# Kernel tuning notes

Measured on AMD Instinct MI355X. Metric: run time of the kernel, lower is better.

The kernel has to match this reference:

```python
import jax, jax.numpy as jnp
import numpy as np

B, T, C, HR = 8, 4096, 256, 4
N_LAYER, LAYER_ID = 12, 3
HID = HR * C


def _fancy_decay_first():
    # Faithful reproduction of VRWKV_SpatialMix._init_weights(init_mode='fancy')
    r01 = LAYER_ID / (N_LAYER - 1)
    h = np.arange(C, dtype=np.float32)
    decay = -5.0 + 8.0 * (h / (C - 1)) ** (0.7 + 1.3 * r01)
    zig = ((np.arange(1, C + 1) % 3) - 1).astype(np.float32) * 0.5
    first = np.float32(np.log(0.3)) + zig
    return jnp.asarray(decay, jnp.float32), jnp.asarray(first, jnp.float32)


def setup_inputs() -> dict:
    key = jax.random.key(0)
    ks = jax.random.split(key, 12)
    s = 0.02  # small weight scale keeps exp(k) well-conditioned
    decay, first = _fancy_decay_first()
    return {
        "x": jax.random.normal(ks[0], (B, T, C), jnp.float32),
        "Wk": jax.random.normal(ks[1], (C, C), jnp.float32) * s,
        "Wv": jax.random.normal(ks[2], (C, C), jnp.float32) * s,
        "Wr": jax.random.normal(ks[3], (C, C), jnp.float32) * s,
        "Wo": jax.random.normal(ks[4], (C, C), jnp.float32) * s,
        "Wk_ffn": jax.random.normal(ks[5], (C, HID), jnp.float32) * s,
        "Wv_ffn": jax.random.normal(ks[6], (HID, C), jnp.float32) * s,
        "Wr_ffn": jax.random.normal(ks[7], (C, C), jnp.float32) * s,
        "g1": 1.0 + 0.1 * jax.random.normal(ks[8], (C,), jnp.float32),
        "b1": 0.1 * jax.random.normal(ks[9], (C,), jnp.float32),
        "g2": 1.0 + 0.1 * jax.random.normal(ks[10], (C,), jnp.float32),
        "b2": 0.1 * jax.random.normal(ks[11], (C,), jnp.float32),
        "spatial_decay": decay,
        "spatial_first": first,
    }


def _ln(x, g, b):
    m = jnp.mean(x, axis=-1, keepdims=True)
    v = jnp.var(x, axis=-1, keepdims=True)
    return (x - m) * jax.lax.rsqrt(v + 1e-5) * g + b


def _wkv(w, u, k, v):
    # Numerically-stable log-space WKV recurrence (same math as wkv_cuda):
    # y_t = (sum_{i<t} e^{w*(t-1-i)+k_i} v_i + e^{u+k_t} v_t)
    #     / (sum_{i<t} e^{w*(t-1-i)+k_i}     + e^{u+k_t})
    # w,u: [C]; k,v: [B,T,C] -> y: [B,T,C]
    Bb, Tt, Cc = k.shape
    kT = jnp.swapaxes(k, 0, 1)  # [T,B,C]
    vT = jnp.swapaxes(v, 0, 1)

    def step(carry, kv):
        p, q, o = carry           # [B,C] num / den / running max exponent
        kt, vt = kv               # [B,C]
        no = jnp.maximum(o, u + kt)
        A = jnp.exp(o - no)
        E = jnp.exp(u + kt - no)
        y = (A * p + E * vt) / (A * q + E)
        no2 = jnp.maximum(w + o, kt)
        A2 = jnp.exp(w + o - no2)
        E2 = jnp.exp(kt - no2)
        return (A2 * p + E2 * vt, A2 * q + E2, no2), y

    init = (jnp.zeros((Bb, Cc), k.dtype),
            jnp.zeros((Bb, Cc), k.dtype),
            jnp.full((Bb, Cc), -1e38, k.dtype))
    _, yT = jax.lax.scan(step, init, (kT, vT))
    return jnp.swapaxes(yT, 0, 1)


def reference(x, Wk, Wv, Wr, Wo, Wk_ffn, Wv_ffn, Wr_ffn, g1, b1, g2, b2,
              spatial_decay, spatial_first):
    Tlen = x.shape[1]
    # --- SpatialMix (shift_pixel=0 -> xk=xv=xr=h, key_norm=False) ---
    h = _ln(x, g1, b1)
    k = h @ Wk
    v = h @ Wv
    sr = jax.nn.sigmoid(h @ Wr)
    y = _wkv(spatial_decay / Tlen, spatial_first / Tlen, k, v)
    x = x + (sr * y) @ Wo
    # --- ChannelMix (square-ReLU MLP, sigmoid receptance gate) ---
    h2 = _ln(x, g2, b2)
    kk = jnp.square(jax.nn.relu(h2 @ Wk_ffn))
    x = x + jax.nn.sigmoid(h2 @ Wr_ffn) * (kk @ Wv_ffn)
    return x
```

## Files before the change

kernel.cpp:

```cpp
#include <hip/hip_runtime.h>
#include <hip/hip_bf16.h>
#include <math.h>

#define TDIM 4096
#define CDIM 256
#define BDIM 8
#define NTOK (BDIM * TDIM)
#define HIDDIM 1024
#define NCHUNK 256
#define CHLEN 16

typedef float f32x4 __attribute__((ext_vector_type(4)));
typedef __bf16 bf16x8 __attribute__((ext_vector_type(8)));
typedef __bf16 bf16x4 __attribute__((ext_vector_type(4)));
typedef long long i64x2 __attribute__((ext_vector_type(2)));

#define GLDS16(gp, lp) __builtin_amdgcn_global_load_lds( \
    (const __attribute__((address_space(1))) void*)(gp), \
    (__attribute__((address_space(3))) void*)(lp), 16, 0, 0)

#define WAITCNT_VM5  0x0F75
#define WAITCNT_VM4  0x0F74
#define WAITCNT_VM0  0x0F70

__device__ __forceinline__ float sigm(float v) { return 1.0f / (1.0f + __expf(-v)); }

__device__ __forceinline__ int permk(int k) {
  return (k & ~63) + (((k >> 3) & 3) << 4) + (((k >> 5) & 1) << 3) + (k & 7);
}

__global__ __launch_bounds__(256) void pack_weights(
    const float* __restrict__ Wk, const float* __restrict__ Wv,
    const float* __restrict__ Wr, const float* __restrict__ Wo,
    const float* __restrict__ Wkf, const float* __restrict__ Wvf,
    const float* __restrict__ Wrf,
    __bf16* __restrict__ WoT, unsigned char* __restrict__ Wkvr8,
    unsigned char* __restrict__ Wkfr8, unsigned char* __restrict__ Wvf8) {
  long long j = (long long)blockIdx.x * 256 + threadIdx.x;
  if (j < 49152) {
    const long long d = j * 4;
    const int n = (int)(d >> 8), k0 = (int)(d & 255);
    const float* src = (n < 256) ? Wk : (n < 512 ? Wv : Wr);
    const int nn = n & 255;
    int w = 0;
    w = __builtin_amdgcn_cvt_pk_fp8_f32(src[k0 * 256 + nn],
                                        src[(k0 + 1) * 256 + nn], w, false);
    w = __builtin_amdgcn_cvt_pk_fp8_f32(src[(k0 + 2) * 256 + nn],
                                        src[(k0 + 3) * 256 + nn], w, true);
    *(int*)&Wkvr8[(long long)n * 256 + permk(k0)] = w;
    return;
  }
  j -= 49152;
  if (j < 65536) { int n = (int)(j >> 8), k = (int)(j & 255);
    WoT[j] = (__bf16)Wo[k * 256 + n]; return; }
  j -= 65536;
  if (j < 81920) {
    const long long d = j * 4;
    const int n = (int)(d >> 8), k0 = (int)(d & 255);
    float v0, v1, v2, v3;
    if (n < 1024) {
      v0 = Wkf[(long long)k0 * 1024 + n];       v1 = Wkf[(long long)(k0 + 1) * 1024 + n];
      v2 = Wkf[(long long)(k0 + 2) * 1024 + n]; v3 = Wkf[(long long)(k0 + 3) * 1024 + n];
    } else {
      const int m = n - 1024;
      v0 = Wrf[k0 * 256 + m];       v1 = Wrf[(k0 + 1) * 256 + m];
      v2 = Wrf[(k0 + 2) * 256 + m]; v3 = Wrf[(k0 + 3) * 256 + m];
    }
    int w = 0;
    w = __builtin_amdgcn_cvt_pk_fp8_f32(v0, v1, w, false);
    w = __builtin_amdgcn_cvt_pk_fp8_f32(v2, v3, w, true);
    *(int*)&Wkfr8[(long long)n * 256 + permk(k0)] = w;
    return;
  }
  j -= 81920;
  if (j < 65536) {
    const long long d = j * 4;
    const int n = (int)(d >> 10), k0 = (int)(d & 1023);
    int w = 0;
    w = __builtin_amdgcn_cvt_pk_fp8_f32(Wvf[(long long)k0 * 256 + n],
                                        Wvf[(long long)(k0 + 1) * 256 + n], w, false);
    w = __builtin_amdgcn_cvt_pk_fp8_f32(Wvf[(long long)(k0 + 2) * 256 + n],
                                        Wvf[(long long)(k0 + 3) * 256 + n], w, true);
    *(int*)&Wvf8[(long long)n * 1024 + permk(k0)] = w;
    return;
  }
}

__global__ __launch_bounds__(256) void ln_kernel(
    const float* __restrict__ x, const float* __restrict__ gamma,
    const float* __restrict__ beta, unsigned char* __restrict__ h8) {
  const int wave = threadIdx.x >> 6, lane = threadIdx.x & 63;
  const long long row = (long long)blockIdx.x * 4 + wave;
  const long long base = row * CDIM + lane * 4;
  const f32x4 v = *(const f32x4*)&x[base];
  float s = v[0] + v[1] + v[2] + v[3];
  float s2 = v[0]*v[0] + v[1]*v[1] + v[2]*v[2] + v[3]*v[3];
  #pragma unroll
  for (int o = 1; o < 64; o <<= 1) { s += __shfl_xor(s, o); s2 += __shfl_xor(s2, o); }
  const float mean = s * (1.0f / CDIM);
  const float var = s2 * (1.0f / CDIM) - mean * mean;
  const float rstd = rsqrtf(var + 1e-5f);
  const f32x4 g4 = *(const f32x4*)&gamma[lane * 4];
  const f32x4 b4 = *(const f32x4*)&beta[lane * 4];
  float o0 = (v[0] - mean) * rstd * g4[0] + b4[0];
  float o1 = (v[1] - mean) * rstd * g4[1] + b4[1];
  float o2 = (v[2] - mean) * rstd * g4[2] + b4[2];
  float o3 = (v[3] - mean) * rstd * g4[3] + b4[3];
  int w = 0;
  w = __builtin_amdgcn_cvt_pk_fp8_f32(o0, o1, w, false);
  w = __builtin_amdgcn_cvt_pk_fp8_f32(o2, o3, w, true);
  *(int*)&h8[row * CDIM + permk(lane * 4)] = w;
}

template <int K, int EPI>
__global__ __launch_bounds__(256, 3) void gemm9(
    const unsigned char* __restrict__ A8, const unsigned char* __restrict__ B8,
    int M, __bf16* __restrict__ outH, __bf16* __restrict__ outH2,
    unsigned char* __restrict__ outC,
    float* __restrict__ outF, const __bf16* __restrict__ srcH,
    const __bf16* __restrict__ gate) {
  constexpr int NIT = K / 64;
  __shared__ unsigned char sA[3][128 * 64];
  __shared__ unsigned char sB[3][128 * 64];
  const int tid = threadIdx.x;
  const int wave = tid >> 6, lane = tid & 63;
  const int quad = lane >> 4, mrow = lane & 15;
  const long long bm = (long long)blockIdx.x * 128;
  const long long bn = (long long)blockIdx.y * 128;
  const int wm = (wave & 1) * 64, wn = (wave >> 1) * 64;
  const int srow = lane >> 2;
  const int o16 = (lane & 3) * 16;

  auto issue = [&](int g) {
    const int buf = g % 3;
    const long long k0 = (long long)g * 64;
    const int a0 = wave * 32;
    GLDS16(A8 + (bm + a0 + srow) * (long long)K + k0 + o16, &sA[buf][a0 * 64]);
    GLDS16(A8 + (bm + a0 + 16 + srow) * (long long)K + k0 + o16, &sA[buf][(a0 + 16) * 64]);
    GLDS16(B8 + (bn + a0 + srow) * (long long)K + k0 + o16, &sB[buf][a0 * 64]);
    GLDS16(B8 + (bn + a0 + 16 + srow) * (long long)K + k0 + o16, &sB[buf][(a0 + 16) * 64]);
  };

  f32x4 acc[4][4] = {};
  issue(0);
  if (NIT > 1) issue(1);

  auto compute = [&](int g) {
    const int buf = g % 3;
    i64x2 fa[4], fb[4];
    #pragma unroll
    for (int mt = 0; mt < 4; mt++)
      fa[mt] = *(const i64x2*)&sA[buf][(wm + mt * 16 + mrow) * 64 + quad * 16];
    #pragma unroll
    for (int nt = 0; nt < 4; nt++)
      fb[nt] = *(const i64x2*)&sB[buf][(wn + nt * 16 + mrow) * 64 + quad * 16];
    #pragma unroll
    for (int c = 0; c < 2; c++)
      #pragma unroll
      for (int mt = 0; mt < 4; mt++)
        #pragma unroll
        for (int nt = 0; nt < 4; nt++)
          acc[mt][nt] = __builtin_amdgcn_mfma_f32_16x16x32_fp8_fp8(
              fb[nt][c], fa[mt][c], acc[mt][nt], 0, 0, 0);
  };

  #pragma unroll 1
  for (int g = 0; g < NIT; g++) {
    if (g == NIT - 1) {
      __builtin_amdgcn_s_waitcnt(WAITCNT_VM0);
    } else {
      __builtin_amdgcn_s_waitcnt(WAITCNT_VM4);
    }
    __builtin_amdgcn_s_barrier();
    if (g + 2 < NIT) issue(g + 2);
    compute(g);
  }

  #pragma unroll
  for (int mt = 0; mt < 4; mt++) {
    #pragma unroll
    for (int nt = 0; nt < 4; nt++) {
      const long long row = bm + wm + mt * 16 + mrow;
      const long long colb = bn + wn + nt * 16 + quad * 4;
      const f32x4 a = acc[mt][nt];
      if (EPI == 0) {
        const int plane = blockIdx.y >> 1;
        __bf16* o = outH + (long long)plane * ((long long)M * 256);
        const long long c2 = colb & 255;
        bf16x4 v;
        if (plane == 2) {
          #pragma unroll
          for (int r = 0; r < 4; r++) v[r] = (__bf16)sigm(a[r]);
        } else {
          #pragma unroll
          for (int r = 0; r < 4; r++) v[r] = (__bf16)a[r];
        }
        *(bf16x4*)&o[row * 256 + c2] = v;
      } else if (EPI == 2) {
        if (blockIdx.y < 8) {
          float t0 = a[0] > 0.0f ? a[0] : 0.0f;
          float t1 = a[1] > 0.0f ? a[1] : 0.0f;
          float t2 = a[2] > 0.0f ? a[2] : 0.0f;
          float t3 = a[3] > 0.0f ? a[3] : 0.0f;
          int w = 0;
          w = __builtin_amdgcn_cvt_pk_fp8_f32(t0 * t0, t1 * t1, w, false);
          w = __builtin_amdgcn_cvt_pk_fp8_f32(t2 * t2, t3 * t3, w, true);
          *(int*)&outC[row * 1024 + permk((int)colb)] = w;
        } else {
          bf16x4 v;
          #pragma unroll
          for (int r = 0; r < 4; r++) v[r] = (__bf16)sigm(a[r]);
          *(bf16x4*)&outH2[row * 256 + (colb - 1024)] = v;
        }
      } else {
        const long long idx = row * 256 + colb;
        const bf16x4 s4 = *(const bf16x4*)&srcH[idx];
        const bf16x4 g4 = *(const bf16x4*)&gate[idx];
        f32x4 v;
        #pragma unroll
        for (int r = 0; r < 4; r++) v[r] = (float)s4[r] + (float)g4[r] * a[r];
        *(f32x4*)&outF[idx] = v;
      }
    }
  }
}

__global__ __launch_bounds__(256, 2) void gemm7(
    const __bf16* __restrict__ A, const __bf16* __restrict__ Bt,
    const float* __restrict__ x,
    const float* __restrict__ gammaP, const float* __restrict__ betaP,
    __bf16* __restrict__ x1h, unsigned char* __restrict__ h28) {
  constexpr int K = 256;
  __shared__ __bf16 sA[3][64 * 32];
  __shared__ __bf16 sB[3][256 * 32];
  __shared__ float redS[4][64], redQ[4][64];

  const int tid = threadIdx.x;
  const int wave = tid >> 6, lane = tid & 63;
  const int quad = lane >> 4, mrow = lane & 15;
  const long long bm = (long long)blockIdx.x * 64;
  const int wn = wave * 64;
  const int lrow = lane >> 2;
  const int lk = (lane & 3) * 8;

  auto issue = [&](int g) {
    const int buf = g % 3;
    const long long k0 = (long long)g * 32;
    GLDS16(A + (bm + wave * 16 + lrow) * (long long)K + k0 + lk,
           &sA[buf][(wave * 16) * 32]);
    #pragma unroll
    for (int bc = 0; bc < 4; bc++) {
      const int r0 = wave * 64 + bc * 16;
      GLDS16(Bt + (r0 + lrow) * (long long)K + k0 + lk, &sB[buf][r0 * 32]);
    }
  };

  f32x4 acc[4][4] = {};

  auto compute = [&](int g) {
    const int buf = g % 3;
    bf16x8 fa[4], fb[4];
    #pragma unroll
    for (int mt = 0; mt < 4; mt++)
      fa[mt] = *(const bf16x8*)&sA[buf][(mt * 16 + mrow) * 32 + quad * 8];
    #pragma unroll
    for (int nt = 0; nt < 4; nt++)
      fb[nt] = *(const bf16x8*)&sB[buf][(wn + nt * 16 + mrow) * 32 + quad * 8];
    #pragma unroll
    for (int mt = 0; mt < 4; mt++)
      #pragma unroll
      for (int nt = 0; nt < 4; nt++)
        acc[mt][nt] = __builtin_amdgcn_mfma_f32_16x16x32_bf16(fb[nt], fa[mt], acc[mt][nt], 0, 0, 0);
  };

  issue(0);
  issue(1);
  #pragma unroll 1
  for (int g = 0; g < 8; g++) {
    if (g == 7) {
      __builtin_amdgcn_s_waitcnt(WAITCNT_VM0);
    } else {
      __builtin_amdgcn_s_waitcnt(WAITCNT_VM5);
    }
    __builtin_amdgcn_s_barrier();
    if (g + 2 < 8) issue(g + 2);
    compute(g);
  }

  float sum[4] = {0, 0, 0, 0}, sq[4] = {0, 0, 0, 0};
  #pragma unroll
  for (int mt = 0; mt < 4; mt++) {
    #pragma unroll
    for (int nt = 0; nt < 4; nt++) {
      const long long row = bm + mt * 16 + mrow;
      const long long colb = wn + nt * 16 + quad * 4;
      acc[mt][nt] += *(const f32x4*)&x[row * 256 + colb];
      #pragma unroll
      for (int r = 0; r < 4; r++) {
        sum[mt] += acc[mt][nt][r];
        sq[mt] += acc[mt][nt][r] * acc[mt][nt][r];
      }
    }
  }
  #pragma unroll
  for (int mt = 0; mt < 4; mt++) {
    sum[mt] += __shfl_xor(sum[mt], 16); sq[mt] += __shfl_xor(sq[mt], 16);
    sum[mt] += __shfl_xor(sum[mt], 32); sq[mt] += __shfl_xor(sq[mt], 32);
  }
  if (quad == 0) {
    #pragma unroll
    for (int mt = 0; mt < 4; mt++) {
      redS[wave][mt * 16 + mrow] = sum[mt];
      redQ[wave][mt * 16 + mrow] = sq[mt];
    }
  }
  __syncthreads();
  #pragma unroll
  for (int mt = 0; mt < 4; mt++) {
    const int rb = mt * 16 + mrow;
    const float ts = redS[0][rb] + redS[1][rb] + redS[2][rb] + redS[3][rb];
    const float tq = redQ[0][rb] + redQ[1][rb] + redQ[2][rb] + redQ[3][rb];
    const float mean = ts * (1.0f / 256.0f);
    const float rstd = rsqrtf(tq * (1.0f / 256.0f) - mean * mean + 1e-5f);
    const long long row = bm + rb;
    #pragma unroll
    for (int nt = 0; nt < 4; nt++) {
      const long long colb = wn + nt * 16 + quad * 4;
      const f32x4 g4 = *(const f32x4*)&gammaP[colb];
      const f32x4 b4 = *(const f32x4*)&betaP[colb];
      bf16x4 xo;
      const float t0 = acc[mt][nt][0], t1 = acc[mt][nt][1];
      const float t2 = acc[mt][nt][2], t3 = acc[mt][nt][3];
      xo[0] = (__bf16)t0; xo[1] = (__bf16)t1; xo[2] = (__bf16)t2; xo[3] = (__bf16)t3;
      const float h0 = (t0 - mean) * rstd * g4[0] + b4[0];
      const float h1 = (t1 - mean) * rstd * g4[1] + b4[1];
      const float h2v = (t2 - mean) * rstd * g4[2] + b4[2];
      const float h3 = (t3 - mean) * rstd * g4[3] + b4[3];
      *(bf16x4*)&x1h[row * 256 + colb] = xo;
      int w = 0;
      w = __builtin_amdgcn_cvt_pk_fp8_f32(h0, h1, w, false);
      w = __builtin_amdgcn_cvt_pk_fp8_f32(h2v, h3, w, true);
      *(int*)&h28[row * 256 + permk((int)colb)] = w;
    }
  }
}

__global__ __launch_bounds__(256) void wkv_phase1(
    const __bf16* __restrict__ ka, const __bf16* __restrict__ va,
    const float* __restrict__ decay,
    float* __restrict__ Sloc, float* __restrict__ Zloc) {
  const int wave = threadIdx.x >> 6, lane = threadIdx.x & 63;
  const int gi = blockIdx.x * 4 + wave;
  const int b = gi >> 8, chunk = gi & (NCHUNK - 1);
  const int c0 = lane * 4;
  const f32x4 w4 = *(const f32x4*)&decay[c0];
  f32x4 ew;
  #pragma unroll
  for (int r = 0; r < 4; r++) ew[r] = __expf(w4[r] * (1.0f / TDIM));
  f32x4 S = {0,0,0,0}, Z = {0,0,0,0};
  long long base = ((long long)b * TDIM + (long long)chunk * CHLEN) * 256 + c0;
  #pragma unroll 4
  for (int t = 0; t < CHLEN; t++) {
    const bf16x4 k4 = *(const bf16x4*)&ka[base + (long long)t * 256];
    const bf16x4 v4 = *(const bf16x4*)&va[base + (long long)t * 256];
    #pragma unroll
    for (int r = 0; r < 4; r++) {
      const float ek = __expf((float)k4[r]);
      S[r] = ew[r] * S[r] + ek * (float)v4[r];
      Z[r] = ew[r] * Z[r] + ek;
    }
  }
  const long long o = (long long)gi * 256 + c0;
  *(f32x4*)&Sloc[o] = S;
  *(f32x4*)&Zloc[o] = Z;
}

__global__ __launch_bounds__(256) void wkv_phase2(
    const float* __restrict__ Sloc, const float* __restrict__ Zloc,
    const float* __restrict__ decay,
    float* __restrict__ Sstart, float* __restrict__ Zstart) {
  const int idx = blockIdx.x * 256 + threadIdx.x;
  const int c = idx & 255;
  const int b = idx >> 8;
  const float w = decay[c] * (1.0f / TDIM);
  const float ewL = __expf(w * (float)CHLEN);
  float S = 0.0f, Z = 0.0f;
  for (int j = 0; j < NCHUNK; j++) {
    const long long o = ((long long)b * NCHUNK + j) * 256 + c;
    Sstart[o] = S;
    Zstart[o] = Z;
    S = ewL * S + Sloc[o];
    Z = ewL * Z + Zloc[o];
  }
}

__global__ __launch_bounds__(256) void wkv_phase3(
    const __bf16* __restrict__ ka, const __bf16* __restrict__ va,
    const __bf16* __restrict__ ra,
    const float* __restrict__ decay, const float* __restrict__ first,
    const float* __restrict__ Sstart, const float* __restrict__ Zstart,
    __bf16* __restrict__ a2) {
  const int wave = threadIdx.x >> 6, lane = threadIdx.x & 63;
  const int gi = blockIdx.x * 4 + wave;
  const int b = gi >> 8, chunk = gi & (NCHUNK - 1);
  const int c0 = lane * 4;
  const f32x4 w4 = *(const f32x4*)&decay[c0];
  const f32x4 u4 = *(const f32x4*)&first[c0];
  f32x4 ew, eu;
  #pragma unroll
  for (int r = 0; r < 4; r++) {
    ew[r] = __expf(w4[r] * (1.0f / TDIM));
    eu[r] = __expf(u4[r] * (1.0f / TDIM));
  }
  const long long so = (long long)gi * 256 + c0;
  f32x4 S = *(const f32x4*)&Sstart[so];
  f32x4 Z = *(const f32x4*)&Zstart[so];
  long long base = ((long long)b * TDIM + (long long)chunk * CHLEN) * 256 + c0;
  #pragma unroll 2
  for (int t = 0; t < CHLEN; t++) {
    const long long p = base + (long long)t * 256;
    const bf16x4 k4 = *(const bf16x4*)&ka[p];
    const bf16x4 v4 = *(const bf16x4*)&va[p];
    const bf16x4 r4 = *(const bf16x4*)&ra[p];
    bf16x4 o;
    #pragma unroll
    for (int r = 0; r < 4; r++) {
      const float ek = __expf((float)k4[r]);
      const float E = eu[r] * ek;
      const float y = (S[r] + E * (float)v4[r]) / (Z[r] + E);
      o[r] = (__bf16)((float)r4[r] * y);
      S[r] = ew[r] * S[r] + ek * (float)v4[r];
      Z[r] = ew[r] * Z[r] + ek;
    }
    *(bf16x4*)&a2[p] = o;
  }
}

extern "C" void kernel_launch(void* const* d_in, const int* in_sizes, int n_in,
                              void* d_out, int out_size, void* d_ws, size_t ws_size,
                              hipStream_t stream) {
  const float* x     = (const float*)d_in[0];
  const float* Wk    = (const float*)d_in[1];
  const float* Wv    = (const float*)d_in[2];
  const float* Wr    = (const float*)d_in[3];
  const float* Wo    = (const float*)d_in[4];
  const float* Wkf   = (const float*)d_in[5];
  const float* Wvf   = (const float*)d_in[6];
  const float* Wrf   = (const float*)d_in[7];
  const float* g1    = (const float*)d_in[8];
  const float* b1    = (const float*)d_in[9];
  const float* g2    = (const float*)d_in[10];
  const float* b2    = (const float*)d_in[11];
  const float* decay = (const float*)d_in[12];
  const float* first = (const float*)d_in[13];
  float* out = (float*)d_out;
  char* ws = (char*)d_ws;

  __bf16* ka     = (__bf16*)(ws + 0);
  __bf16* va     = (__bf16*)(ws + 16777216LL);
  __bf16* ra     = (__bf16*)(ws + 33554432LL);
  __bf16* a2     = (__bf16*)(ws + 50331648LL);
  __bf16* g2buf  = (__bf16*)(ws + 50331648LL);
  unsigned char* h8  = (unsigned char*)(ws + 67108864LL);
  unsigned char* h28 = (unsigned char*)(ws + 67108864LL);
  __bf16* x1h    = (__bf16*)(ws + 83886080LL);
  unsigned char* kk8 = (unsigned char*)(ws + 100663296LL);
  float*  Sloc   = (float*)(ws + 134217728LL);
  float*  Zloc   = (float*)(ws + 137363456LL);
  float*  Sstart = (float*)(ws + 140509184LL);
  float*  Zstart = (float*)(ws + 143654912LL);
  __bf16* WoT    = (__bf16*)(ws + 167772160LL);
  unsigned char* Wkvr8 = (unsigned char*)(ws + 167903232LL);
  unsigned char* Wkfr8 = (unsigned char*)(ws + 168099840LL);
  unsigned char* Wvf8  = (unsigned char*)(ws + 168427520LL);

  pack_weights<<<1024, 256, 0, stream>>>(Wk, Wv, Wr, Wo, Wkf, Wvf, Wrf,
                                         WoT, Wkvr8, Wkfr8, Wvf8);

  ln_kernel<<<NTOK / 4, 256, 0, stream>>>(x, g1, b1, h8);
  gemm9<256, 0><<<dim3(NTOK / 128, 6), 256, 0, stream>>>(
      h8, Wkvr8, NTOK, ka, nullptr, nullptr, nullptr, nullptr, nullptr);
  wkv_phase1<<<BDIM * NCHUNK / 4, 256, 0, stream>>>(ka, va, decay, Sloc, Zloc);
  wkv_phase2<<<BDIM, 256, 0, stream>>>(Sloc, Zloc, decay, Sstart, Zstart);
  wkv_phase3<<<BDIM * NCHUNK / 4, 256, 0, stream>>>(ka, va, ra, decay, first,
                                                    Sstart, Zstart, a2);
  gemm7<<<NTOK / 64, 256, 0, stream>>>(a2, WoT, x, g2, b2, x1h, h28);

  gemm9<256, 2><<<dim3(NTOK / 128, 10), 256, 0, stream>>>(
      h28, Wkfr8, NTOK, nullptr, g2buf, kk8, nullptr, nullptr, nullptr);
  gemm9<1024, 3><<<dim3(NTOK / 128, 2), 256, 0, stream>>>(
      kk8, Wvf8, NTOK, nullptr, nullptr, nullptr, out, x1h, g2buf);
}
```

Measured before the change: 252.6 us.

## Add persistent fp8 GEMM with register-resident B and double-buffered A tiles

Adds a persistent 512-thread GEMM kernel for the two K=256 projections (QKV/receptance and FFN key/receptance). Each block walks a contiguous range of 128-row tiles, keeps the B fragments in registers and reloads them only when the output column block changes. The next A tile is prefetched into a double-buffered LDS slot while the current one is computed. This targets the launch overhead and the repeated B loads of the one-tile-per-block gemm9 grid, at the cost of higher register pressure and a serialized loop over tiles inside each block.

```diff
diff --git a/kernel.cpp b/kernel.cpp
--- a/kernel.cpp
+++ b/kernel.cpp
@@ -19,6 +19,7 @@
     (const __attribute__((address_space(1))) void*)(gp), \
     (__attribute__((address_space(3))) void*)(lp), 16, 0, 0)
 
+#define WAITCNT_VM8  0x0F78
 #define WAITCNT_VM5  0x0F75
 #define WAITCNT_VM4  0x0F74
 #define WAITCNT_VM0  0x0F70
@@ -110,6 +111,141 @@
   w = __builtin_amdgcn_cvt_pk_fp8_f32(o0, o1, w, false);
   w = __builtin_amdgcn_cvt_pk_fp8_f32(o2, o3, w, true);
   *(int*)&h8[row * CDIM + permk(lane * 4)] = w;
+}
+
+template <int EPI, int NY>
+__global__ __launch_bounds__(512, 4) void gemmF(
+    const unsigned char* __restrict__ A8, const unsigned char* __restrict__ B8,
+    __bf16* __restrict__ outH, __bf16* __restrict__ outH2,
+    unsigned char* __restrict__ outC) {
+  constexpr int NTILES = 256 * NY;
+  constexpr int TPB = NTILES / 512;
+  static_assert(NTILES % 512 == 0, "grid divisibility");
+  __shared__ unsigned char sA[2][4 * 8192];
+
+  const int tid = threadIdx.x;
+  const int wave = tid >> 6, lane = tid & 63;
+  const int quad = lane >> 4, mrow = lane & 15;
+  const int wm = (wave & 1) * 64, wn = (wave >> 1) * 32;
+  const int srow = lane >> 2;
+  const int o16 = (lane & 3) * 16;
+  const int t0 = blockIdx.x * TPB;
+
+  auto issueA = [&](int t, int buf) {
+    const long long bm = (long long)(t & 255) * 128;
+    const int r0 = wave * 16;
+    #pragma unroll
+    for (int g = 0; g < 4; g++)
+      GLDS16(A8 + (bm + r0 + srow) * 256 + g * 64 + o16,
+             &sA[buf][g * 8192 + r0 * 64]);
+  };
+
+  i64x2 fb[2][4];
+  auto loadB = [&](int y) {
+    const long long bn = (long long)y * 128;
+    #pragma unroll
+    for (int nt = 0; nt < 2; nt++)
+      #pragma unroll
+      for (int g = 0; g < 4; g++)
+        fb[nt][g] = *(const i64x2*)
+            &B8[(bn + wn + nt * 16 + mrow) * 256 + g * 64 + quad * 16];
+  };
+
+  issueA(t0, 0);
+  int prevy = -1;
+
+  #pragma unroll 1
+  for (int i = 0; i < TPB; i++) {
+    const int t = t0 + i;
+    const int y = t >> 8;
+    const bool ych = (y != prevy);
+    prevy = y;
+
+    if (i == 0) __builtin_amdgcn_s_waitcnt(WAITCNT_VM0);
+    else        __builtin_amdgcn_s_waitcnt(WAITCNT_VM8);
+    __builtin_amdgcn_s_barrier();
+
+    if (ych) loadB(y);
+    if (i + 1 < TPB) issueA(t + 1, (i + 1) & 1);
+    if (ych) __builtin_amdgcn_s_waitcnt(WAITCNT_VM8);
+
+    f32x4 acc[4][2] = {};
+    const int buf = i & 1;
+    #pragma unroll
+    for (int g = 0; g < 4; g++) {
+      i64x2 fa[4];
+      #pragma unroll
+      for (int mt = 0; mt < 4; mt++)
+        fa[mt] = *(const i64x2*)
+            &sA[buf][g * 8192 + (wm + mt * 16 + mrow) * 64 + quad * 16];
+      #pragma unroll
+      for (int c = 0; c < 2; c++)
+        #pragma unroll
+        for (int mt = 0; mt < 4; mt++)
+          #pragma unroll
+          for (int nt = 0; nt < 2; nt++)
+            acc[mt][nt] = __builtin_amdgcn_mfma_f32_16x16x32_fp8_fp8(
+                fb[nt][g][c], fa[mt][c], acc[mt][nt], 0, 0, 0);
+    }
+
+    const long long bm = (long long)(t & 255) * 128;
+    if (EPI == 0) {
+      const int plane = y >> 1;
+      __bf16* o = outH + (long long)plane * (32768LL * 256);
+      const int cb = (y & 1) * 128 + wn + quad * 4;
+      #pragma unroll
+      for (int mt = 0; mt < 4; mt++) {
+        const long long row = bm + wm + mt * 16 + mrow;
+        #pragma unroll
+        for (int nt = 0; nt < 2; nt++) {
+          const f32x4 a = acc[mt][nt];
+          bf16x4 v;
+          if (plane == 2) {
+            #pragma unroll
+            for (int r = 0; r < 4; r++) v[r] = (__bf16)sigm(a[r]);
+          } else {
+            #pragma unroll
+            for (int r = 0; r < 4; r++) v[r] = (__bf16)a[r];
+          }
+          *(bf16x4*)&o[row * 256 + cb + nt * 16] = v;
+        }
+      }
+    } else {
+      if (y < 8) {
+        const int cb = y * 128 + wn + quad * 4;
+        #pragma unroll
+        for (int mt = 0; mt < 4; mt++) {
+          const long long row = bm + wm + mt * 16 + mrow;
+          #pragma unroll
+          for (int nt = 0; nt < 2; nt++) {
+            const f32x4 a = acc[mt][nt];
+            float q0 = a[0] > 0.0f ? a[0] : 0.0f;
+            float q1 = a[1] > 0.0f ? a[1] : 0.0f;
+            float q2 = a[2] > 0.0f ? a[2] : 0.0f;
+            float q3 = a[3] > 0.0f ? a[3] : 0.0f;
+            int w = 0;
+            w = __builtin_amdgcn_cvt_pk_fp8_f32(q0 * q0, q1 * q1, w, false);
+            w = __builtin_amdgcn_cvt_pk_fp8_f32(q2 * q2, q3 * q3, w, true);
+            *(int*)&outC[row * 1024 + permk(cb + nt * 16)] = w;
+          }
+        }
+      } else {
+        const int cb = (y - 8) * 128 + wn + quad * 4;
+        #pragma unroll
+        for (int mt = 0; mt < 4; mt++) {
+          const long long row = bm + wm + mt * 16 + mrow;
+          #pragma unroll
+          for (int nt = 0; nt < 2; nt++) {
+            const f32x4 a = acc[mt][nt];
+            bf16x4 v;
+            #pragma unroll
+            for (int r = 0; r < 4; r++) v[r] = (__bf16)sigm(a[r]);
+            *(bf16x4*)&outH2[row * 256 + cb + nt * 16] = v;
+          }
+        }
+      }
+    }
+  }
 }
 
 template <int K, int EPI>
@@ -478,16 +614,14 @@
                                          WoT, Wkvr8, Wkfr8, Wvf8);
 
   ln_kernel<<<NTOK / 4, 256, 0, stream>>>(x, g1, b1, h8);
-  gemm9<256, 0><<<dim3(NTOK / 128, 6), 256, 0, stream>>>(
-      h8, Wkvr8, NTOK, ka, nullptr, nullptr, nullptr, nullptr, nullptr);
+  gemmF<0, 6><<<512, 512, 0, stream>>>(h8, Wkvr8, ka, nullptr, nullptr);
   wkv_phase1<<<BDIM * NCHUNK / 4, 256, 0, stream>>>(ka, va, decay, Sloc, Zloc);
   wkv_phase2<<<BDIM, 256, 0, stream>>>(Sloc, Zloc, decay, Sstart, Zstart);
   wkv_phase3<<<BDIM * NCHUNK / 4, 256, 0, stream>>>(ka, va, ra, decay, first,
                                                     Sstart, Zstart, a2);
   gemm7<<<NTOK / 64, 256, 0, stream>>>(a2, WoT, x, g2, b2, x1h, h28);
 
-  gemm9<256, 2><<<dim3(NTOK / 128, 10), 256, 0, stream>>>(
-      h28, Wkfr8, NTOK, nullptr, g2buf, kk8, nullptr, nullptr, nullptr);
+  gemmF<2, 10><<<512, 512, 0, stream>>>(h28, Wkfr8, nullptr, g2buf, kk8);
   gemm9<1024, 3><<<dim3(NTOK / 128, 2), 256, 0, stream>>>(
       kk8, Wvf8, NTOK, nullptr, nullptr, nullptr, out, x1h, g2buf);
 }
```

New measurement: 255.7 us. No clear change (+1.2%).
